# Optimization experiments

Hardware: AMD Instinct MI355X
Metric: run time of the kernel (lower is better)

The kernel has to match this reference:

```python
import jax, jax.numpy as jnp
import numpy as np

BLOCK, HALO, HEADS = 8, 3, 4


def setup_inputs() -> dict:
    key = jax.random.key(0)
    k1, k2, k3, k4 = jax.random.split(key, 4)
    ch, d = 128, 128 // HEADS
    win = BLOCK + 2 * HALO
    return {
        "x": jax.random.normal(k1, (8, ch, 128, 128), dtype=jnp.float32),
        "qkv_w": jax.random.normal(k2, (3 * ch, ch), dtype=jnp.float32) * (2.0 / ch) ** 0.5,
        "rel_h": jax.random.normal(k3, (1, win, 1, d // 2), dtype=jnp.float32),
        "rel_w": jax.random.normal(k4, (1, 1, win, d // 2), dtype=jnp.float32),
    }


def _halo_windows(t, block, halo):
    b, c, h, w = t.shape
    win = block + 2 * halo
    nh, nw = h // block, w // block
    tp = jnp.pad(t, ((0, 0), (0, 0), (halo, halo), (halo, halo)))
    idx_h = (jnp.arange(nh) * block)[:, None] + jnp.arange(win)[None, :]
    idx_w = (jnp.arange(nw) * block)[:, None] + jnp.arange(win)[None, :]
    return tp[:, :, idx_h[:, None, :, None], idx_w[None, :, None, :]]


def reference(x, qkv_w, rel_h, rel_w):
    block, halo, heads = BLOCK, HALO, HEADS
    b, c, h, w = x.shape
    d = c // heads
    win = block + 2 * halo
    nh, nw = h // block, w // block

    # 1x1 conv (bias=False)
    qkv = jnp.einsum('bchw,oc->bohw', x, qkv_w)
    q, k, v = jnp.split(qkv, 3, axis=1)

    # q: non-overlapping blocks -> (b, nh, nw, heads, block*block, d), scaled
    q = q.reshape(b, heads, d, nh, block, nw, block)
    q = q.transpose(0, 3, 5, 1, 4, 6, 2).reshape(b, nh, nw, heads, block * block, d)
    q = q * d ** -0.5

    kw = _halo_windows(k, block, halo)
    vw = _halo_windows(v, block, halo)
    kw = kw.reshape(b, heads, d, nh, nw, win, win).transpose(0, 3, 4, 1, 5, 6, 2)
    vw = vw.reshape(b, heads, d, nh, nw, win, win).transpose(0, 3, 4, 1, 5, 6, 2)
    vw = vw.reshape(b, nh, nw, heads, win * win, d)

    # relative position bias added to keys (first half varies over rows, second over cols)
    k_h, k_w2 = jnp.split(kw, 2, axis=-1)
    kw = jnp.concatenate([k_h + rel_h, k_w2 + rel_w], axis=-1)
    kw = kw.reshape(b, nh, nw, heads, win * win, d)

    sim = jnp.einsum('...id,...jd->...ij', q, kw)
    attn = jax.nn.softmax(sim, axis=-1)
    out = jnp.einsum('...ij,...jd->...id', attn, vw)  # (b,nh,nw,heads, blk^2, d)

    # reassemble: channel = (head, d) head-major; rows = (nh, k1); cols = (nw, k2)
    out = out.reshape(b, nh, nw, heads, block, block, d)
    out = out.transpose(0, 3, 6, 1, 4, 2, 5).reshape(b, c, h, w)
    return out
```

## Files before the change

kernel.cpp:

```cpp
#include <hip/hip_runtime.h>
#include <hip/hip_bf16.h>


typedef __attribute__((ext_vector_type(8))) short bf16x8;
typedef __attribute__((ext_vector_type(4))) short bf16x4;
typedef __attribute__((ext_vector_type(4))) float f32x4;
union BF8 { bf16x8 v; unsigned u[4]; };
union BF4 { bf16x4 v; unsigned u[2]; };

#define DEVI static __device__ __forceinline__

DEVI short f2bf(float f) {
    __bf16 h = (__bf16)f;
    union { __bf16 h; short s; } c; c.h = h; return c.s;
}
DEVI unsigned pk2(float a, float b) {
    return (unsigned)(unsigned short)f2bf(a) | ((unsigned)(unsigned short)f2bf(b) << 16);
}

#if defined(__has_builtin)
#  if __has_builtin(__builtin_amdgcn_mfma_f32_16x16x16bf16_1k)
#    define HAVE_MFMA16_1K 1
#  endif
#endif

DEVI f32x4 mfma16(bf16x4 a, bf16x4 b, f32x4 c) {
#ifdef HAVE_MFMA16_1K
    return __builtin_amdgcn_mfma_f32_16x16x16bf16_1k(a, b, c, 0, 0, 0);
#else
    f32x4 d;
    asm("v_mfma_f32_16x16x16_bf16 %0, %1, %2, %3" : "=v"(d) : "v"(a), "v"(b), "v"(c));
    return d;
#endif
}

#define QSCALE (0.17677669529663687f * 1.4426950408889634f)

__global__ void wcvt(const float* __restrict__ w, short* __restrict__ ws_w) {
    int e = blockIdx.x * 256 + threadIdx.x;
    if (e < 384 * 128) {
        float v = w[e];
        if (e < 128 * 128) v *= QSCALE;
        ws_w[e] = f2bf(v);
    }
}

__launch_bounds__(256)
__global__ void qkv_gemm(const float* __restrict__ x, const short* __restrict__ ws_w,
                         short* __restrict__ ws_q, short* __restrict__ ws_k,
                         short* __restrict__ ws_v) {
    const int blk = blockIdx.x;
    const int b = blk >> 6;
    const int pixbase = (blk & 63) << 8;
    const int tid = threadIdx.x, wv = tid >> 6, ln = tid & 63;
    const int lr = ln & 15, lg = ln >> 4;
    const int n0 = pixbase + wv * 64;
    const f32x4 zz = {0.f, 0.f, 0.f, 0.f};

    BF8 Bx[4][4];
    #pragma unroll
    for (int nt = 0; nt < 4; ++nt) {
        const int pix = n0 + nt * 16 + lr;
        #pragma unroll
        for (int ks = 0; ks < 4; ++ks) {
            const float* xp = x + (((size_t)((b << 7) + ks * 32 + lg * 8)) << 14) + pix;
            float f[8];
            #pragma unroll
            for (int e = 0; e < 8; ++e) f[e] = xp[(size_t)e << 14];
            Bx[nt][ks].u[0] = pk2(f[0], f[1]); Bx[nt][ks].u[1] = pk2(f[2], f[3]);
            Bx[nt][ks].u[2] = pk2(f[4], f[5]); Bx[nt][ks].u[3] = pk2(f[6], f[7]);
        }
    }

    for (int ot = 0; ot < 24; ++ot) {
        bf16x8 Aw[4];
        #pragma unroll
        for (int ks = 0; ks < 4; ++ks)
            Aw[ks] = *(const bf16x8*)&ws_w[(ot * 16 + lr) * 128 + ks * 32 + lg * 8];
        f32x4 acc[4];
        #pragma unroll
        for (int nt = 0; nt < 4; ++nt) {
            acc[nt] = zz;
            #pragma unroll
            for (int ks = 0; ks < 4; ++ks)
                acc[nt] = __builtin_amdgcn_mfma_f32_16x16x32_bf16(Aw[ks], Bx[nt][ks].v, acc[nt], 0, 0, 0);
        }
        if (ot < 8) {
            const int head = ot >> 1, dd0 = ((ot & 1) << 4) + lg * 4;
            #pragma unroll
            for (int nt = 0; nt < 4; ++nt) {
                const int pix = n0 + nt * 16 + lr;
                const int gr = pix >> 7, gc = pix & 127;
                const int ii = gr >> 3, jj = gc >> 3;
                const int qrow = ((gr & 7) << 3) | (gc & 7);
                size_t off = ((size_t)((((b * 16 + ii) * 16 + jj) << 2) + head) << 11) + qrow * 32 + dd0;
                *(uint2*)&ws_q[off] = make_uint2(pk2(acc[nt][0], acc[nt][1]), pk2(acc[nt][2], acc[nt][3]));
            }
        } else if (ot < 16) {
            const int head = (ot - 8) >> 1, dd0 = (((ot - 8) & 1) << 4) + lg * 4;
            const size_t kb = ((size_t)(b * 4 + head)) << 19;
            #pragma unroll
            for (int nt = 0; nt < 4; ++nt) {
                const int pix = n0 + nt * 16 + lr;
                *(uint2*)&ws_k[kb + pix * 32 + dd0] =
                    make_uint2(pk2(acc[nt][0], acc[nt][1]), pk2(acc[nt][2], acc[nt][3]));
            }
        } else {
            const int vch = ((ot - 16) << 4) + lg * 4;
            const int head = vch >> 5, dd = vch & 31;
            #pragma unroll
            for (int nt = 0; nt < 4; ++nt) {
                const int pix = n0 + nt * 16 + lr;
                const int gr = pix >> 7, gc = pix & 127;
                const size_t base = ((((size_t)(b * 4 + head) << 7) + gr) * 32 + dd) * 136 + 3 + gc;
                #pragma unroll
                for (int r = 0; r < 4; ++r) ws_v[base + r * 136] = f2bf(acc[nt][r]);
            }
        }
    }
}

template<bool EDGE>
DEVI void attn_body(int b, int i, int j, int head, int ln,
                    const short* __restrict__ ws_q, const short* __restrict__ ws_k,
                    const short* __restrict__ ws_v,
                    const float* __restrict__ rel_h, const float* __restrict__ rel_w,
                    float* __restrict__ out) {
    const int lr = ln & 15, lg = ln >> 4;
    const f32x4 zz = {0.f, 0.f, 0.f, 0.f};
    const int bh = b * 4 + head;

    const short* qbase = ws_q + ((size_t)((((b * 16 + i) * 16 + j) << 2) + head) << 11);
    const short* kbase = ws_k + (((size_t)bh) << 19);
    const short* vbase = ws_v + (size_t)bh * (128 * 32 * 136);

    bf16x8 Bq[4];
    #pragma unroll
    for (int mt = 0; mt < 4; ++mt)
        Bq[mt] = *(const bf16x8*)&qbase[(mt * 16 + lr) * 32 + lg * 8];

    BF8 Ah, Awf;
    #pragma unroll
    for (int wd = 0; wd < 4; ++wd) { Ah.u[wd] = 0u; Awf.u[wd] = 0u; }
    if (lr < 14) {
        if (lg < 2) {
            const float* rp = rel_h + lr * 16 + lg * 8;
            #pragma unroll
            for (int wd = 0; wd < 4; ++wd) Ah.u[wd] = pk2(rp[2 * wd], rp[2 * wd + 1]);
        } else {
            const float* rp = rel_w + lr * 16 + (lg - 2) * 8;
            #pragma unroll
            for (int wd = 0; wd < 4; ++wd) Awf.u[wd] = pk2(rp[2 * wd], rp[2 * wd + 1]);
        }
    }
    f32x4 qh4[4], qw4[4];
    #pragma unroll
    for (int mt = 0; mt < 4; ++mt) {
        qh4[mt] = __builtin_amdgcn_mfma_f32_16x16x32_bf16(Ah.v, Bq[mt], zz, 0, 0, 0);
        qw4[mt] = __builtin_amdgcn_mfma_f32_16x16x32_bf16(Awf.v, Bq[mt], zz, 0, 0, 0);
    }
    if (lg == 3) {
        #pragma unroll
        for (int mt = 0; mt < 4; ++mt) { qw4[mt][2] = -16384.f; qw4[mt][3] = -16384.f; }
    }

    BF4 Bones; Bones.u[0] = 0x3F803F80u; Bones.u[1] = 0x3F803F80u;

    f32x4 a0[4] = {zz, zz, zz, zz}, a1[4] = {zz, zz, zz, zz}, sA[4] = {zz, zz, zz, zz};
    #pragma unroll
    for (int t = 0; t < 14; ++t) {
        const int gr = i * 8 - 3 + t;
        const int gc = j * 8 - 3 + lr;
        const int grc = EDGE ? min(max(gr, 0), 127) : gr;
        BF8 Ak;
        if (EDGE) {
            const int gcc = min(max(gc, 0), 127);
            Ak.v = *(const bf16x8*)&kbase[((grc << 7) + gcc) * 32 + lg * 8];
            if (gr != grc || gc != gcc) { Ak.u[0] = 0; Ak.u[1] = 0; Ak.u[2] = 0; Ak.u[3] = 0; }
        } else {
            Ak.v = *(const bf16x8*)&kbase[((gr << 7) + gc) * 32 + lg * 8];
        }

        const int colb = j * 8 + lg * 4;
        BF4 Bv0, Bv1;
        *(uint2*)Bv0.u = *(const uint2*)&vbase[((grc << 5) + lr) * 136 + colb];
        *(uint2*)Bv1.u = *(const uint2*)&vbase[((grc << 5) + 16 + lr) * 136 + colb];
        if (EDGE) {
            const int gc0 = colb - 3;
            const int lo = max(0, -gc0), hi = min(3, 127 - gc0);
            const unsigned bits = ((unsigned)gr < 128u && lo <= hi)
                                ? (((0xFu >> (3 - (hi - lo))) << lo) & 0xFu) : 0u;
            const unsigned mm0 = ((bits & 1u) ? 0x0000FFFFu : 0u) | ((bits & 2u) ? 0xFFFF0000u : 0u);
            const unsigned mm1 = ((bits & 4u) ? 0x0000FFFFu : 0u) | ((bits & 8u) ? 0xFFFF0000u : 0u);
            Bv0.u[0] &= mm0; Bv0.u[1] &= mm1; Bv1.u[0] &= mm0; Bv1.u[1] &= mm1;
        }

        #pragma unroll
        for (int mt = 0; mt < 4; ++mt) {
            const float qh = __shfl(qh4[mt][t & 3], ((t >> 2) << 4) | lr, 64);
            f32x4 cin;
            #pragma unroll
            for (int r = 0; r < 4; ++r) cin[r] = qw4[mt][r] + qh;
            const f32x4 p = __builtin_amdgcn_mfma_f32_16x16x32_bf16(Ak.v, Bq[mt], cin, 0, 0, 0);
            BF4 Ap;
            Ap.u[0] = pk2(exp2f(p[0]), exp2f(p[1]));
            Ap.u[1] = pk2(exp2f(p[2]), exp2f(p[3]));
            a0[mt] = mfma16(Ap.v, Bv0.v, a0[mt]);
            a1[mt] = mfma16(Ap.v, Bv1.v, a1[mt]);
            sA[mt] = mfma16(Ap.v, Bones.v, sA[mt]);
        }
    }

    #pragma unroll
    for (int mt = 0; mt < 4; ++mt) {
        f32x4 acc0, acc1;
        #pragma unroll
        for (int r = 0; r < 4; ++r) {
            const float rinv = __builtin_amdgcn_rcpf(sA[mt][r]);
            acc0[r] = a0[mt][r] * rinv;
            acc1[r] = a1[mt][r] * rinv;
        }
        const int qb = mt * 16 + lg * 4;
        float* op = out + (((size_t)(b * 128 + head * 32)) << 14)
                        + ((i * 8 + (qb >> 3)) << 7) + j * 8 + (qb & 7);
        *(f32x4*)(op + ((size_t)lr << 14)) = acc0;
        *(f32x4*)(op + ((size_t)(16 + lr) << 14)) = acc1;
    }
}

__launch_bounds__(256)
__global__ void attn3(const short* __restrict__ ws_q, const short* __restrict__ ws_k,
                      const short* __restrict__ ws_v,
                      const float* __restrict__ rel_h, const float* __restrict__ rel_w,
                      float* __restrict__ out) {
    const int bid = blockIdx.x;
    const int blk = ((bid & 7) << 8) | (bid >> 3);
    const int j = blk & 15, i = (blk >> 4) & 15, b = blk >> 8;
    const int head = threadIdx.x >> 6, ln = threadIdx.x & 63;
    if (i == 0 || i == 15 || j == 0 || j == 15)
        attn_body<true>(b, i, j, head, ln, ws_q, ws_k, ws_v, rel_h, rel_w, out);
    else
        attn_body<false>(b, i, j, head, ln, ws_q, ws_k, ws_v, rel_h, rel_w, out);
}

__launch_bounds__(256, 2)
__global__ void halo_attn(const float* __restrict__ x,
                          const float* __restrict__ qkv_w,
                          const float* __restrict__ relh_g,
                          const float* __restrict__ relw_g,
                          float* __restrict__ out)
{
    const int blk  = blockIdx.x;
    const int head = blk & 3;
    const int j    = (blk >> 2) & 15;
    const int i    = (blk >> 6) & 15;
    const int b    = blk >> 10;
    const int tid = threadIdx.x;
    const int wv  = tid >> 6;
    const int ln  = tid & 63;
    const int lr  = ln & 15;
    const int lg  = ln >> 4;

    __shared__ __align__(16) union { short xs[112*128]; short pbuf[64*224]; } XP;
    __shared__ __align__(16) short kbuf[208*32];
    __shared__ __align__(16) short vbufT[32*224];
    __shared__ __align__(16) short qbuf[64*32];
    __shared__ float smax[4*64];
    __shared__ float ssum[4*64];
    __shared__ float relh[224];
    __shared__ float relw[224];

    for (int t = tid; t < 32*224/2; t += 256) ((int*)vbufT)[t] = 0;
    for (int t = tid; t < 224; t += 256) { relh[t] = relh_g[t]; relw[t] = relw_g[t]; }

    bf16x8 Bw[6][4];
    #pragma unroll
    for (int n = 0; n < 6; ++n) {
        const int obase = (n < 2) ? head*32 + n*16
                        : (n < 4) ? 128 + head*32 + (n-2)*16
                                  : 256 + head*32 + (n-4)*16;
        const float* wp0 = qkv_w + (obase + lr)*128;
        #pragma unroll
        for (int ks = 0; ks < 4; ++ks) {
            const float* wp = wp0 + ks*32 + lg*8;
            bf16x8 f;
            #pragma unroll
            for (int e = 0; e < 8; ++e) f[e] = f2bf(wp[e]);
            Bw[n][ks] = f;
        }
    }

    for (int ph = 0; ph < 2; ++ph) {
        __syncthreads();
        for (int t = tid; t < 112*128; t += 256) {
            const int ch = t / 112;
            const int p  = t - ch*112;
            float val = 0.f;
            if (p < 98) {
                const int P  = ph*98 + p;
                const int wr = P / 14, wc = P - wr*14;
                const int gr = i*8 - 3 + wr, gc = j*8 - 3 + wc;
                if ((unsigned)gr < 128u && (unsigned)gc < 128u)
                    val = x[((b*128 + ch)*128 + gr)*128 + gc];
            }
            XP.xs[p*128 + (ch & 7) + 8*((ch >> 3) ^ (p & 15))] = f2bf(val);
        }
        __syncthreads();

        for (int mt = wv; mt < 7; mt += 4) {
            const int row = mt*16 + lr;
            bf16x8 A[4];
            #pragma unroll
            for (int ks = 0; ks < 4; ++ks)
                A[ks] = *(const bf16x8*)&XP.xs[row*128 + 8*((ks*4 + lg) ^ (row & 15))];
            #pragma unroll
            for (int n = 0; n < 6; ++n) {
                f32x4 acc = {0.f, 0.f, 0.f, 0.f};
                #pragma unroll
                for (int ks = 0; ks < 4; ++ks)
                    acc = __builtin_amdgcn_mfma_f32_16x16x32_bf16(A[ks], Bw[n][ks], acc, 0, 0, 0);
                #pragma unroll
                for (int r = 0; r < 4; ++r) {
                    const int p = mt*16 + lg*4 + r;
                    if (p >= 98) continue;
                    const int P  = ph*98 + p;
                    const int wr = P / 14, wc = P - wr*14;
                    const float val = acc[r];
                    if (n < 2) {
                        if (wr >= 3 && wr <= 10 && wc >= 3 && wc <= 10) {
                            const int qi = (wr-3)*8 + (wc-3);
                            const int dd = n*16 + lr;
                            qbuf[qi*32 + (dd & 7) + 8*((dd >> 3) ^ ((qi >> 1) & 3))] =
                                f2bf(val * 0.17677669529663687f);
                        }
                    } else if (n < 4) {
                        const int dd = (n-2)*16 + lr;
                        const float bias = (dd < 16) ? relh[wr*16 + dd] : relw[wc*16 + dd - 16];
                        kbuf[P*32 + (dd & 7) + 8*((dd >> 3) ^ ((P >> 1) & 3))] = f2bf(val + bias);
                    } else {
                        const int dd = (n-4)*16 + lr;
                        vbufT[dd*224 + (P & 7) + 8*((P >> 3) ^ ((dd >> 1) & 3))] = f2bf(val);
                    }
                }
            }
        }
    }
    __syncthreads();

    bf16x8 Aq[4];
    #pragma unroll
    for (int mt = 0; mt < 4; ++mt) {
        const int row = mt*16 + lr;
        Aq[mt] = *(const bf16x8*)&qbuf[row*32 + 8*(lg ^ ((row >> 1) & 3))];
    }

    f32x4 sim[4][4];
    #pragma unroll
    for (int ntl = 0; ntl < 4; ++ntl) {
        const int nt = wv + ntl*4;
        if (nt > 12) continue;
        const int P = nt*16 + lr;
        const bf16x8 Bk = *(const bf16x8*)&kbuf[P*32 + 8*(lg ^ ((P >> 1) & 3))];
        #pragma unroll
        for (int mt = 0; mt < 4; ++mt) {
            const f32x4 z = {0.f, 0.f, 0.f, 0.f};
            sim[ntl][mt] = __builtin_amdgcn_mfma_f32_16x16x32_bf16(Aq[mt], Bk, z, 0, 0, 0);
        }
    }

    for (int t = tid; t < 64*224/2; t += 256) ((int*)XP.pbuf)[t] = 0;

    #pragma unroll
    for (int mt = 0; mt < 4; ++mt)
    #pragma unroll
    for (int r = 0; r < 4; ++r) {
        float m = -1e30f;
        #pragma unroll
        for (int ntl = 0; ntl < 4; ++ntl) {
            const int nt = wv + ntl*4;
            if (nt > 12) continue;
            const int key = nt*16 + lr;
            if (key < 196) m = fmaxf(m, sim[ntl][mt][r]);
        }
        #pragma unroll
        for (int off = 1; off < 16; off <<= 1)
            m = fmaxf(m, __shfl_xor(m, off, 64));
        if (lr == 0) smax[wv*64 + mt*16 + lg*4 + r] = m;
    }
    __syncthreads();

    #pragma unroll
    for (int mt = 0; mt < 4; ++mt)
    #pragma unroll
    for (int r = 0; r < 4; ++r) {
        const int qrow = mt*16 + lg*4 + r;
        const float gm = fmaxf(fmaxf(smax[qrow], smax[64+qrow]),
                               fmaxf(smax[128+qrow], smax[192+qrow]));
        float s = 0.f;
        #pragma unroll
        for (int ntl = 0; ntl < 4; ++ntl) {
            const int nt = wv + ntl*4;
            if (nt > 12) continue;
            const int key = nt*16 + lr;
            float e = (key < 196) ? __expf(sim[ntl][mt][r] - gm) : 0.f;
            sim[ntl][mt][r] = e;
            s += e;
        }
        #pragma unroll
        for (int off = 1; off < 16; off <<= 1)
            s += __shfl_xor(s, off, 64);
        if (lr == 0) ssum[wv*64 + qrow] = s;
    }
    __syncthreads();

    #pragma unroll
    for (int mt = 0; mt < 4; ++mt)
    #pragma unroll
    for (int r = 0; r < 4; ++r) {
        const int qrow = mt*16 + lg*4 + r;
        const float rinv = 1.f / (ssum[qrow] + ssum[64+qrow] + ssum[128+qrow] + ssum[192+qrow]);
        #pragma unroll
        for (int ntl = 0; ntl < 4; ++ntl) {
            const int nt = wv + ntl*4;
            if (nt > 12) continue;
            const int key = nt*16 + lr;
            XP.pbuf[qrow*224 + (key & 7) + 8*((key >> 3) ^ ((qrow >> 1) & 3))] =
                f2bf(sim[ntl][mt][r] * rinv);
        }
    }
    __syncthreads();

    f32x4 oacc[2] = {{0.f,0.f,0.f,0.f},{0.f,0.f,0.f,0.f}};
    const int mt = wv;
    #pragma unroll
    for (int ks = 0; ks < 7; ++ks) {
        const int row = mt*16 + lr;
        const int g = ks*4 + lg;
        const bf16x8 Ap = *(const bf16x8*)&XP.pbuf[row*224 + 8*(g ^ ((row >> 1) & 3))];
        #pragma unroll
        for (int n = 0; n < 2; ++n) {
            const int dd = n*16 + lr;
            const bf16x8 Bv = *(const bf16x8*)&vbufT[dd*224 + 8*(g ^ ((dd >> 1) & 3))];
            oacc[n] = __builtin_amdgcn_mfma_f32_16x16x32_bf16(Ap, Bv, oacc[n], 0, 0, 0);
        }
    }

    #pragma unroll
    for (int n = 0; n < 2; ++n) {
        const int dd = n*16 + lr;
        const int c  = head*32 + dd;
        const int qb = mt*16 + lg*4;
        const int rb = qb >> 3, cb = qb & 7;
        float* op = out + ((b*128 + c)*128 + (i*8 + rb))*128 + j*8 + cb;
        *(f32x4*)op = oacc[n];
    }
}

extern "C" void kernel_launch(void* const* d_in, const int* in_sizes, int n_in,
                              void* d_out, int out_size, void* d_ws, size_t ws_size,
                              hipStream_t stream)
{
    const float* x  = (const float*)d_in[0];
    const float* w  = (const float*)d_in[1];
    const float* rh = (const float*)d_in[2];
    const float* rw = (const float*)d_in[3];
    float* o = (float*)d_out;

    const size_t Q_ELEMS = (size_t)8192 * 2048;
    const size_t K_ELEMS = (size_t)32 * 16384 * 32;
    const size_t V_ELEMS = (size_t)32 * 128 * 32 * 136;
    const size_t W_ELEMS = (size_t)384 * 128;
    const size_t NEED = (Q_ELEMS + K_ELEMS + V_ELEMS + W_ELEMS) * 2 + 1024;

    if (ws_size >= NEED) {
        short* ws_q = (short*)d_ws;
        short* ws_k = ws_q + Q_ELEMS;
        short* ws_v = ws_k + K_ELEMS;
        short* ws_w = ws_v + V_ELEMS;
        wcvt<<<dim3(192), dim3(256), 0, stream>>>(w, ws_w);
        qkv_gemm<<<dim3(512), dim3(256), 0, stream>>>(x, ws_w, ws_q, ws_k, ws_v);
        attn3<<<dim3(2048), dim3(256), 0, stream>>>(ws_q, ws_k, ws_v, rh, rw, o);
    } else {
        halo_attn<<<dim3(8192), dim3(256), 0, stream>>>(x, w, rh, rw, o);
    }
}
```

Before: 122.4 us.

## Split attention query tiles across two blocks and hoist edge masks out of loop

```diff
diff --git a/kernel.cpp b/kernel.cpp
--- a/kernel.cpp
+++ b/kernel.cpp
@@ -121,7 +121,7 @@
 }
 
 template<bool EDGE>
-DEVI void attn_body(int b, int i, int j, int head, int ln,
+DEVI void attn_body(int b, int i, int j, int head, int ln, int mt0,
                     const short* __restrict__ ws_q, const short* __restrict__ ws_k,
                     const short* __restrict__ ws_v,
                     const float* __restrict__ rel_h, const float* __restrict__ rel_w,
@@ -134,10 +134,10 @@
     const short* kbase = ws_k + (((size_t)bh) << 19);
     const short* vbase = ws_v + (size_t)bh * (128 * 32 * 136);
 
-    bf16x8 Bq[4];
-    #pragma unroll
-    for (int mt = 0; mt < 4; ++mt)
-        Bq[mt] = *(const bf16x8*)&qbase[(mt * 16 + lr) * 32 + lg * 8];
+    bf16x8 Bq[2];
+    #pragma unroll
+    for (int m = 0; m < 2; ++m)
+        Bq[m] = *(const bf16x8*)&qbase[((mt0 + m) * 16 + lr) * 32 + lg * 8];
 
     BF8 Ah, Awf;
     #pragma unroll
@@ -153,74 +153,78 @@
             for (int wd = 0; wd < 4; ++wd) Awf.u[wd] = pk2(rp[2 * wd], rp[2 * wd + 1]);
         }
     }
-    f32x4 qh4[4], qw4[4];
-    #pragma unroll
-    for (int mt = 0; mt < 4; ++mt) {
-        qh4[mt] = __builtin_amdgcn_mfma_f32_16x16x32_bf16(Ah.v, Bq[mt], zz, 0, 0, 0);
-        qw4[mt] = __builtin_amdgcn_mfma_f32_16x16x32_bf16(Awf.v, Bq[mt], zz, 0, 0, 0);
+    f32x4 qh4[2], qw4[2];
+    #pragma unroll
+    for (int m = 0; m < 2; ++m) {
+        qh4[m] = __builtin_amdgcn_mfma_f32_16x16x32_bf16(Ah.v, Bq[m], zz, 0, 0, 0);
+        qw4[m] = __builtin_amdgcn_mfma_f32_16x16x32_bf16(Awf.v, Bq[m], zz, 0, 0, 0);
     }
     if (lg == 3) {
         #pragma unroll
-        for (int mt = 0; mt < 4; ++mt) { qw4[mt][2] = -16384.f; qw4[mt][3] = -16384.f; }
+        for (int m = 0; m < 2; ++m) { qw4[m][2] = -16384.f; qw4[m][3] = -16384.f; }
     }
 
     BF4 Bones; Bones.u[0] = 0x3F803F80u; Bones.u[1] = 0x3F803F80u;
 
-    f32x4 a0[4] = {zz, zz, zz, zz}, a1[4] = {zz, zz, zz, zz}, sA[4] = {zz, zz, zz, zz};
+    const int gc   = j * 8 - 3 + lr;
+    const int gcc  = EDGE ? min(max(gc, 0), 127) : gc;
+    const bool gcBad = EDGE && (gc != gcc);
+    const int colb = j * 8 + lg * 4;
+    unsigned mmc0 = 0xFFFFFFFFu, mmc1 = 0xFFFFFFFFu;
+    if (EDGE) {
+        const int gc0 = colb - 3;
+        const int lo = max(0, -gc0), hi = min(3, 127 - gc0);
+        const unsigned bits = (lo <= hi) ? (((0xFu >> (3 - (hi - lo))) << lo) & 0xFu) : 0u;
+        mmc0 = ((bits & 1u) ? 0x0000FFFFu : 0u) | ((bits & 2u) ? 0xFFFF0000u : 0u);
+        mmc1 = ((bits & 4u) ? 0x0000FFFFu : 0u) | ((bits & 8u) ? 0xFFFF0000u : 0u);
+    }
+
+    f32x4 a0[2] = {zz, zz}, a1[2] = {zz, zz}, sA[2] = {zz, zz};
     #pragma unroll
     for (int t = 0; t < 14; ++t) {
         const int gr = i * 8 - 3 + t;
-        const int gc = j * 8 - 3 + lr;
+        const bool grOK = !EDGE || ((unsigned)gr < 128u);
         const int grc = EDGE ? min(max(gr, 0), 127) : gr;
+
         BF8 Ak;
-        if (EDGE) {
-            const int gcc = min(max(gc, 0), 127);
-            Ak.v = *(const bf16x8*)&kbase[((grc << 7) + gcc) * 32 + lg * 8];
-            if (gr != grc || gc != gcc) { Ak.u[0] = 0; Ak.u[1] = 0; Ak.u[2] = 0; Ak.u[3] = 0; }
-        } else {
-            Ak.v = *(const bf16x8*)&kbase[((gr << 7) + gc) * 32 + lg * 8];
-        }
-
-        const int colb = j * 8 + lg * 4;
+        Ak.v = *(const bf16x8*)&kbase[((grc << 7) + gcc) * 32 + lg * 8];
+        if (EDGE && (gcBad || !grOK)) { Ak.u[0] = 0; Ak.u[1] = 0; Ak.u[2] = 0; Ak.u[3] = 0; }
+
         BF4 Bv0, Bv1;
         *(uint2*)Bv0.u = *(const uint2*)&vbase[((grc << 5) + lr) * 136 + colb];
         *(uint2*)Bv1.u = *(const uint2*)&vbase[((grc << 5) + 16 + lr) * 136 + colb];
         if (EDGE) {
-            const int gc0 = colb - 3;
-            const int lo = max(0, -gc0), hi = min(3, 127 - gc0);
-            const unsigned bits = ((unsigned)gr < 128u && lo <= hi)
-                                ? (((0xFu >> (3 - (hi - lo))) << lo) & 0xFu) : 0u;
-            const unsigned mm0 = ((bits & 1u) ? 0x0000FFFFu : 0u) | ((bits & 2u) ? 0xFFFF0000u : 0u);
-            const unsigned mm1 = ((bits & 4u) ? 0x0000FFFFu : 0u) | ((bits & 8u) ? 0xFFFF0000u : 0u);
+            const unsigned mm0 = grOK ? mmc0 : 0u;
+            const unsigned mm1 = grOK ? mmc1 : 0u;
             Bv0.u[0] &= mm0; Bv0.u[1] &= mm1; Bv1.u[0] &= mm0; Bv1.u[1] &= mm1;
         }
 
         #pragma unroll
-        for (int mt = 0; mt < 4; ++mt) {
-            const float qh = __shfl(qh4[mt][t & 3], ((t >> 2) << 4) | lr, 64);
+        for (int m = 0; m < 2; ++m) {
+            const float qh = __shfl(qh4[m][t & 3], ((t >> 2) << 4) | lr, 64);
             f32x4 cin;
             #pragma unroll
-            for (int r = 0; r < 4; ++r) cin[r] = qw4[mt][r] + qh;
-            const f32x4 p = __builtin_amdgcn_mfma_f32_16x16x32_bf16(Ak.v, Bq[mt], cin, 0, 0, 0);
+            for (int r = 0; r < 4; ++r) cin[r] = qw4[m][r] + qh;
+            const f32x4 p = __builtin_amdgcn_mfma_f32_16x16x32_bf16(Ak.v, Bq[m], cin, 0, 0, 0);
             BF4 Ap;
             Ap.u[0] = pk2(exp2f(p[0]), exp2f(p[1]));
             Ap.u[1] = pk2(exp2f(p[2]), exp2f(p[3]));
-            a0[mt] = mfma16(Ap.v, Bv0.v, a0[mt]);
-            a1[mt] = mfma16(Ap.v, Bv1.v, a1[mt]);
-            sA[mt] = mfma16(Ap.v, Bones.v, sA[mt]);
-        }
-    }
-
-    #pragma unroll
-    for (int mt = 0; mt < 4; ++mt) {
+            a0[m] = mfma16(Ap.v, Bv0.v, a0[m]);
+            a1[m] = mfma16(Ap.v, Bv1.v, a1[m]);
+            sA[m] = mfma16(Ap.v, Bones.v, sA[m]);
+        }
+    }
+
+    #pragma unroll
+    for (int m = 0; m < 2; ++m) {
         f32x4 acc0, acc1;
         #pragma unroll
         for (int r = 0; r < 4; ++r) {
-            const float rinv = __builtin_amdgcn_rcpf(sA[mt][r]);
-            acc0[r] = a0[mt][r] * rinv;
-            acc1[r] = a1[mt][r] * rinv;
-        }
-        const int qb = mt * 16 + lg * 4;
+            const float rinv = __builtin_amdgcn_rcpf(sA[m][r]);
+            acc0[r] = a0[m][r] * rinv;
+            acc1[r] = a1[m][r] * rinv;
+        }
+        const int qb = (mt0 + m) * 16 + lg * 4;
         float* op = out + (((size_t)(b * 128 + head * 32)) << 14)
                         + ((i * 8 + (qb >> 3)) << 7) + j * 8 + (qb & 7);
         *(f32x4*)(op + ((size_t)lr << 14)) = acc0;
@@ -229,18 +233,18 @@
 }
 
 __launch_bounds__(256)
-__global__ void attn3(const short* __restrict__ ws_q, const short* __restrict__ ws_k,
+__global__ void attn4(const short* __restrict__ ws_q, const short* __restrict__ ws_k,
                       const short* __restrict__ ws_v,
                       const float* __restrict__ rel_h, const float* __restrict__ rel_w,
                       float* __restrict__ out) {
     const int bid = blockIdx.x;
-    const int blk = ((bid & 7) << 8) | (bid >> 3);
-    const int j = blk & 15, i = (blk >> 4) & 15, b = blk >> 8;
+    const int blk = ((bid & 7) << 9) | (bid >> 3);
+    const int half = blk & 1, j = (blk >> 1) & 15, i = (blk >> 5) & 15, b = blk >> 9;
     const int head = threadIdx.x >> 6, ln = threadIdx.x & 63;
     if (i == 0 || i == 15 || j == 0 || j == 15)
-        attn_body<true>(b, i, j, head, ln, ws_q, ws_k, ws_v, rel_h, rel_w, out);
+        attn_body<true>(b, i, j, head, ln, half * 2, ws_q, ws_k, ws_v, rel_h, rel_w, out);
     else
-        attn_body<false>(b, i, j, head, ln, ws_q, ws_k, ws_v, rel_h, rel_w, out);
+        attn_body<false>(b, i, j, head, ln, half * 2, ws_q, ws_k, ws_v, rel_h, rel_w, out);
 }
 
 __launch_bounds__(256, 2)
@@ -479,7 +483,7 @@
         short* ws_w = ws_v + V_ELEMS;
         wcvt<<<dim3(192), dim3(256), 0, stream>>>(w, ws_w);
         qkv_gemm<<<dim3(512), dim3(256), 0, stream>>>(x, ws_w, ws_q, ws_k, ws_v);
-        attn3<<<dim3(2048), dim3(256), 0, stream>>>(ws_q, ws_k, ws_v, rh, rw, o);
+        attn4<<<dim3(4096), dim3(256), 0, stream>>>(ws_q, ws_k, ws_v, rh, rw, o);
     } else {
         halo_attn<<<dim3(8192), dim3(256), 0, stream>>>(x, w, rh, rw, o);
     }
```

New measurement: 114.5 us. 1.07x faster.
